# Optimization experiments

Hardware: AMD Instinct MI355X
Metric: run time of the kernel (lower is better)

Reference implementation:

```python
import jax, jax.numpy as jnp
import numpy as np

B, DIM, H, W = 16, 512, 32, 32
C = 256          # internal channels = int(512*0.5)
HEADS = 4        # max(1, 256//64)
KD = 32          # key_dim = int(64*0.5)
HD = 64          # head_dim = 256//4
SCALE = KD ** -0.5


def _silu(x):
    return x * jax.nn.sigmoid(x)


def conv1x1(x, Wm, s, b, act):
    # 1x1 conv + folded eval-mode BN (scale/shift) + optional SiLU
    y = jnp.einsum('bchw,oc->bohw', x, Wm)
    y = y * s[None, :, None, None] + b[None, :, None, None]
    return _silu(y) if act else y


def dwconv3(x, Wd, s, b):
    # depthwise 3x3 conv (groups = channels) + BN scale/shift, no act
    y = jax.lax.conv_general_dilated(
        x, Wd, window_strides=(1, 1), padding='SAME',
        feature_group_count=x.shape[1],
        dimension_numbers=('NCHW', 'OIHW', 'NCHW'))
    return y * s[None, :, None, None] + b[None, :, None, None]


def _mk_conv(key, c_out, c_in, k=1):
    k1, k2, k3 = jax.random.split(key, 3)
    fan_in = c_in * k * k
    if k == 1:
        Wm = jax.random.normal(k1, (c_out, c_in), jnp.float32) * fan_in ** -0.5
    else:
        Wm = jax.random.normal(k1, (c_out, c_in, k, k), jnp.float32) * fan_in ** -0.5
    s = jax.random.uniform(k2, (c_out,), jnp.float32, 0.5, 1.5)
    b = 0.1 * jax.random.normal(k3, (c_out,), jnp.float32)
    return Wm, s, b


def setup_inputs() -> dict:
    key = jax.random.key(0)
    ks = jax.random.split(key, 8)
    x = jax.random.normal(ks[0], (B, DIM, H, W), jnp.float32)
    W_cv1, s_cv1, b_cv1 = _mk_conv(ks[1], 2 * C, DIM)
    W_qkv, s_qkv, b_qkv = _mk_conv(ks[2], C + 2 * HEADS * KD, C)  # 512 out
    W_proj, s_proj, b_proj = _mk_conv(ks[3], C, C)
    # depthwise 3x3: OIHW with I=1, groups=C
    W_pe, s_pe, b_pe = _mk_conv(ks[4], C, 1, k=3)
    W_ffn1, s_ffn1, b_ffn1 = _mk_conv(ks[5], 2 * C, C)
    W_ffn2, s_ffn2, b_ffn2 = _mk_conv(ks[6], C, 2 * C)
    W_cv2, s_cv2, b_cv2 = _mk_conv(ks[7], DIM, 2 * C)
    return {
        'x': x,
        'W_cv1': W_cv1, 's_cv1': s_cv1, 'b_cv1': b_cv1,
        'W_qkv': W_qkv, 's_qkv': s_qkv, 'b_qkv': b_qkv,
        'W_proj': W_proj, 's_proj': s_proj, 'b_proj': b_proj,
        'W_pe': W_pe, 's_pe': s_pe, 'b_pe': b_pe,
        'W_ffn1': W_ffn1, 's_ffn1': s_ffn1, 'b_ffn1': b_ffn1,
        'W_ffn2': W_ffn2, 's_ffn2': s_ffn2, 'b_ffn2': b_ffn2,
        'W_cv2': W_cv2, 's_cv2': s_cv2, 'b_cv2': b_cv2,
    }


def reference(x,
              W_cv1, s_cv1, b_cv1,
              W_qkv, s_qkv, b_qkv,
              W_proj, s_proj, b_proj,
              W_pe, s_pe, b_pe,
              W_ffn1, s_ffn1, b_ffn1,
              W_ffn2, s_ffn2, b_ffn2,
              W_cv2, s_cv2, b_cv2):
    bsz, _, h, w = x.shape
    n = h * w
    y = conv1x1(x, W_cv1, s_cv1, b_cv1, act=True)          # [b, 2C, h, w]
    a, bb = y[:, :C], y[:, C:]

    # ----- Attention on bb -----
    qkv = conv1x1(bb, W_qkv, s_qkv, b_qkv, act=False)       # [b, 2*h*kd + C, h, w]
    qkv = qkv.reshape(bsz, HEADS, 2 * KD + HD, n)
    q, k, v = qkv[:, :, :KD], qkv[:, :, KD:2 * KD], qkv[:, :, 2 * KD:]
    attn = jnp.einsum('bhdn,bhdm->bhnm', q, k) * SCALE      # [b, heads, n, n]
    attn = jax.nn.softmax(attn, axis=-1)
    xa = jnp.einsum('bhdm,bhnm->bhdn', v, attn).reshape(bsz, C, h, w)
    xa = xa + dwconv3(v.reshape(bsz, C, h, w), W_pe, s_pe, b_pe)
    xa = conv1x1(xa, W_proj, s_proj, b_proj, act=False)
    bb = bb + xa

    # ----- FFN on bb -----
    ff = conv1x1(bb, W_ffn1, s_ffn1, b_ffn1, act=True)
    ff = conv1x1(ff, W_ffn2, s_ffn2, b_ffn2, act=False)
    bb = bb + ff

    return conv1x1(jnp.concatenate([a, bb], axis=1), W_cv2, s_cv2, b_cv2, act=True)
```

## Files before the change

kernel.cpp:

```cpp
#include <hip/hip_runtime.h>

typedef unsigned short u16;
typedef __attribute__((ext_vector_type(8))) short short8;
typedef __attribute__((ext_vector_type(4))) float f32x4;
typedef __attribute__((ext_vector_type(4))) unsigned int uint4v;
typedef __attribute__((ext_vector_type(4))) unsigned short ushort4v;

#define N_PIX 1024
constexpr float SCALE = 0.17677669529663687f;
constexpr float QSC   = 0.25506626725324577f;

__device__ __forceinline__ float bf2f(u16 v) {
    unsigned u = ((unsigned)v) << 16;
    return __builtin_bit_cast(float, u);
}
__device__ __forceinline__ u16 f2bf(float f) {
    unsigned u = __builtin_bit_cast(unsigned, f);
    u += 0x7fff + ((u >> 16) & 1);
    return (u16)(u >> 16);
}
__device__ __forceinline__ float silu_f(float x) { return x / (1.f + __expf(-x)); }

__device__ __forceinline__ float exp2_f(float x) {
    float r; asm("v_exp_f32 %0, %1" : "=v"(r) : "v"(x)); return r;
}

__device__ __forceinline__ f32x4 mfma16(short8 a, short8 b, f32x4 c) {
    return __builtin_amdgcn_mfma_f32_16x16x32_bf16(a, b, c, 0, 0, 0);
}

__device__ __forceinline__ void gl_lds16(const u16* g, u16* l) {
    __builtin_amdgcn_global_load_lds(
        (const __attribute__((address_space(1))) unsigned int*)g,
        (__attribute__((address_space(3))) unsigned int*)l, 16, 0, 0);
}

__device__ __forceinline__ float dpp_max16(float x) {
    int v = __builtin_bit_cast(int, x);
    x = fmaxf(x, __builtin_bit_cast(float, __builtin_amdgcn_mov_dpp(v, 0xB1, 0xF, 0xF, true)));
    v = __builtin_bit_cast(int, x);
    x = fmaxf(x, __builtin_bit_cast(float, __builtin_amdgcn_mov_dpp(v, 0x4E, 0xF, 0xF, true)));
    v = __builtin_bit_cast(int, x);
    x = fmaxf(x, __builtin_bit_cast(float, __builtin_amdgcn_mov_dpp(v, 0x141, 0xF, 0xF, true)));
    v = __builtin_bit_cast(int, x);
    x = fmaxf(x, __builtin_bit_cast(float, __builtin_amdgcn_mov_dpp(v, 0x140, 0xF, 0xF, true)));
    return x;
}
__device__ __forceinline__ float dpp_sum16(float x) {
    int v = __builtin_bit_cast(int, x);
    x += __builtin_bit_cast(float, __builtin_amdgcn_mov_dpp(v, 0xB1, 0xF, 0xF, true));
    v = __builtin_bit_cast(int, x);
    x += __builtin_bit_cast(float, __builtin_amdgcn_mov_dpp(v, 0x4E, 0xF, 0xF, true));
    v = __builtin_bit_cast(int, x);
    x += __builtin_bit_cast(float, __builtin_amdgcn_mov_dpp(v, 0x141, 0xF, 0xF, true));
    v = __builtin_bit_cast(int, x);
    x += __builtin_bit_cast(float, __builtin_amdgcn_mov_dpp(v, 0x140, 0xF, 0xF, true));
    return x;
}

__global__ void cvtw_k(const float* s0, u16* d0, int n0,
                       const float* s1, u16* d1, int n1,
                       const float* s2, u16* d2, int n2,
                       const float* s3, u16* d3, int n3,
                       const float* s4, u16* d4, int n4,
                       const float* s5, u16* d5, int n5)
{
    const float* sp = nullptr; u16* dp = nullptr; int n = 0;
    switch (blockIdx.y) {
        case 0: sp = s0; dp = d0; n = n0; break;
        case 1: sp = s1; dp = d1; n = n1; break;
        case 2: sp = s2; dp = d2; n = n2; break;
        case 3: sp = s3; dp = d3; n = n3; break;
        case 4: sp = s4; dp = d4; n = n4; break;
        case 5: sp = s5; dp = d5; n = n5; break;
    }
    for (int i = blockIdx.x * 256 + threadIdx.x; i < n; i += gridDim.x * 256)
        dp[i] = f2bf(sp[i]);
}

__global__ __launch_bounds__(256) void trans_k(const float* __restrict__ x, u16* __restrict__ xt)
{
    __shared__ float LT[64 * 65];
    const int tid = threadIdx.x;
    const int n0 = blockIdx.x * 64;
    const int c0 = blockIdx.y * 64;
    const int b  = blockIdx.z;
    const int w = tid >> 6, ln = tid & 63;
#pragma unroll
    for (int s = 0; s < 16; ++s) {
        int c = s * 4 + w;
        LT[c * 65 + ln] = x[((size_t)(b * 512 + c0 + c)) * N_PIX + n0 + ln];
    }
    __syncthreads();
#pragma unroll
    for (int s = 0; s < 16; ++s) {
        int n = s * 4 + w;
        xt[((size_t)(b * N_PIX + n0 + n)) * 512 + c0 + ln] = f2bf(LT[ln * 65 + n]);
    }
}

__global__ __launch_bounds__(512) void gemm_k(
    const u16* __restrict__ Xt, int xcs, int xcoff,
    const u16* __restrict__ Wb, int Cin,
    const float* __restrict__ sc, const float* __restrict__ bi,
    const u16* __restrict__ res, int rcs, int rcoff,
    u16* __restrict__ out, int ocs, int ocoff,
    float* __restrict__ out32,
    u16* __restrict__ vsep,
    int act)
{
    __shared__ __align__(16) u16 WT[2][128 * 32];
    __shared__ __align__(16) u16 XT[2][128 * 32];
    const int tid  = threadIdx.x;
    const int lane = tid & 63;
    const int w    = __builtin_amdgcn_readfirstlane(tid >> 6);
    const int wr = w & 3;
    const int wc = w >> 2;
    const int n0 = blockIdx.x * 128;
    const int o0 = blockIdx.y * 128;
    const int b  = blockIdx.z;
    const int l4 = lane >> 4, l15 = lane & 15;

    const int srow = tid >> 2;
    const int skc  = (tid & 3) * 8;
    const u16* wg = Wb + (size_t)(o0 + srow) * Cin + skc;
    const u16* xg = Xt + ((size_t)(b * N_PIX + n0 + srow)) * xcs + xcoff + skc;

    f32x4 acc[2][4];
#pragma unroll
    for (int i = 0; i < 2; ++i)
#pragma unroll
        for (int j = 0; j < 4; ++j) acc[i][j] = (f32x4){0.f, 0.f, 0.f, 0.f};

    const int nk = Cin >> 5;
    gl_lds16(wg, &WT[0][tid * 8]);
    gl_lds16(xg, &XT[0][tid * 8]);
    __syncthreads();

    for (int kk = 0; kk < nk; ++kk) {
        const int cur = kk & 1;
        if (kk + 1 < nk) {
            const int cc = (kk + 1) << 5;
            gl_lds16(wg + cc, &WT[cur ^ 1][tid * 8]);
            gl_lds16(xg + cc, &XT[cur ^ 1][tid * 8]);
        }
        short8 af[2], bfr[4];
#pragma unroll
        for (int i = 0; i < 2; ++i)
            af[i] = *(const short8*)&WT[cur][(wr * 32 + i * 16 + l15) * 32 + l4 * 8];
#pragma unroll
        for (int j = 0; j < 4; ++j)
            bfr[j] = *(const short8*)&XT[cur][(wc * 64 + j * 16 + l15) * 32 + l4 * 8];
#pragma unroll
        for (int i = 0; i < 2; ++i)
#pragma unroll
            for (int j = 0; j < 4; ++j)
                acc[i][j] = mfma16(af[i], bfr[j], acc[i][j]);
        __syncthreads();
    }

    if (out32) {
        const int Cout = gridDim.y * 128;
        float* eplds = (float*)XT;
        const int row = tid >> 4, cb = (tid & 15) * 8;
#pragma unroll
        for (int hh = 0; hh < 4; ++hh) {
            if (wr == hh) {
#pragma unroll
                for (int i = 0; i < 2; ++i)
#pragma unroll
                    for (int j = 0; j < 4; ++j)
#pragma unroll
                        for (int r = 0; r < 4; ++r) {
                            const int oo = i * 16 + l4 * 4 + r;
                            const int go = o0 + hh * 32 + oo;
                            float v = acc[i][j][r] * sc[go] + bi[go];
                            if (act) v = silu_f(v);
                            eplds[oo * 128 + wc * 64 + j * 16 + l15] = v;
                        }
            }
            __syncthreads();
            const size_t gidx = ((size_t)b * Cout + o0 + hh * 32 + row) * N_PIX + n0 + cb;
            f32x4 a0 = *(const f32x4*)&eplds[row * 128 + cb];
            f32x4 a1 = *(const f32x4*)&eplds[row * 128 + cb + 4];
            *(f32x4*)&out32[gidx]     = a0;
            *(f32x4*)&out32[gidx + 4] = a1;
            __syncthreads();
        }
        return;
    }

    const bool is_v = (vsep != nullptr) && (wr >= 2);
    const float qmul = (vsep != nullptr && wr == 0) ? QSC : 1.f;
#pragma unroll
    for (int i = 0; i < 2; ++i) {
        const int ob = o0 + wr * 32 + i * 16 + l4 * 4;
        float s4[4], b4[4];
#pragma unroll
        for (int r = 0; r < 4; ++r) { s4[r] = sc[ob + r] * qmul; b4[r] = bi[ob + r] * qmul; }
#pragma unroll
        for (int j = 0; j < 4; ++j) {
            const int n = n0 + wc * 64 + j * 16 + l15;
            float v[4];
#pragma unroll
            for (int r = 0; r < 4; ++r) {
                v[r] = acc[i][j][r] * s4[r] + b4[r];
                if (act) v[r] = silu_f(v[r]);
            }
            if (is_v) {
                const int hh = ob >> 7;
                const int dv = (ob & 127) - 64;
                u16* vp = vsep + (((size_t)(b * 4 + hh)) * 64 + dv) * N_PIX + n;
#pragma unroll
                for (int r = 0; r < 4; ++r) vp[r * N_PIX] = f2bf(v[r]);
            } else {
                const size_t base = ((size_t)(b * N_PIX + n)) * ocs + ocoff + ob;
                if (res) {
                    ushort4v rr = *(const ushort4v*)&res[((size_t)(b * N_PIX + n)) * rcs + rcoff + ob];
#pragma unroll
                    for (int r = 0; r < 4; ++r) v[r] += bf2f(rr[r]);
                }
                ushort4v pk;
#pragma unroll
                for (int r = 0; r < 4; ++r) pk[r] = f2bf(v[r]);
                *(ushort4v*)&out[base] = pk;
            }
        }
    }
}

__global__ __launch_bounds__(256, 4) void attn_k(
    const u16* __restrict__ qkvt, const u16* __restrict__ vsep,
    u16* __restrict__ xat)
{
    __shared__ __align__(16) u16 PL[4 * 16 * 72];
    const int tid  = threadIdx.x;
    const int lane = tid & 63;
    const int w    = __builtin_amdgcn_readfirstlane(tid >> 6);
    const int l4 = lane >> 4, l15 = lane & 15;
    const int h = blockIdx.y, b = blockIdx.z;
    const int n0w = blockIdx.x * 64 + w * 16;
    u16* PLw = PL + w * 16 * 72;

    const short8 qf = *(const short8*)&qkvt[((size_t)(b * N_PIX + n0w + l15)) * 512 + h * 128 + l4 * 8];
    const u16* kb = qkvt + ((size_t)(b * N_PIX + l15)) * 512 + h * 128 + 32 + l4 * 8;
    const u16* vb = vsep + (((size_t)(b * 4 + h)) * 64 + l15) * N_PIX + l4 * 8;

    float mrun[4], lrun[4];
#pragma unroll
    for (int r = 0; r < 4; ++r) { mrun[r] = -1e30f; lrun[r] = 0.f; }
    f32x4 accv[4];
#pragma unroll
    for (int d = 0; d < 4; ++d) accv[d] = (f32x4){0.f, 0.f, 0.f, 0.f};
    const f32x4 z4 = {0.f, 0.f, 0.f, 0.f};

    for (int t = 0; t < 16; ++t) {
        const int m0 = t * 64;
        short8 kf[4];
#pragma unroll
        for (int mt = 0; mt < 4; ++mt)
            kf[mt] = *(const short8*)(kb + (size_t)(m0 + mt * 16) * 512);
        short8 vf[2][4];
#pragma unroll
        for (int mq = 0; mq < 2; ++mq)
#pragma unroll
            for (int d = 0; d < 4; ++d)
                vf[mq][d] = *(const short8*)(vb + (size_t)(d * 16) * N_PIX + m0 + mq * 32);

        f32x4 s[4];
        __builtin_amdgcn_s_setprio(1);
#pragma unroll
        for (int mt = 0; mt < 4; ++mt) s[mt] = mfma16(qf, kf[mt], z4);
        __builtin_amdgcn_s_setprio(0);

        float tm[4], g = -1e30f;
#pragma unroll
        for (int r = 0; r < 4; ++r) {
            float m_ = fmaxf(fmaxf(s[0][r], s[1][r]), fmaxf(s[2][r], s[3][r]));
            tm[r] = dpp_max16(m_);
            g = fmaxf(g, tm[r] - mrun[r]);
        }
        if (!__all(g <= 11.0f)) {
#pragma unroll
            for (int r = 0; r < 4; ++r) {
                float mnew = fmaxf(mrun[r], tm[r]);
                float corr = exp2_f(mrun[r] - mnew);
                mrun[r] = mnew;
                lrun[r] *= corr;
#pragma unroll
                for (int d = 0; d < 4; ++d) accv[d][r] *= corr;
            }
        }
#pragma unroll
        for (int mt = 0; mt < 4; ++mt)
#pragma unroll
            for (int r = 0; r < 4; ++r) {
                float p = exp2_f(s[mt][r] - mrun[r]);
                lrun[r] += p;
                PLw[(l4 * 4 + r) * 72 + mt * 16 + l15] = f2bf(p);
            }

        __builtin_amdgcn_s_setprio(1);
#pragma unroll
        for (int mq = 0; mq < 2; ++mq) {
            short8 pa = *(const short8*)&PLw[l15 * 72 + mq * 32 + l4 * 8];
#pragma unroll
            for (int d = 0; d < 4; ++d)
                accv[d] = mfma16(pa, vf[mq][d], accv[d]);
        }
        __builtin_amdgcn_s_setprio(0);
    }

#pragma unroll
    for (int r = 0; r < 4; ++r)
        lrun[r] = 1.f / dpp_sum16(lrun[r]);
#pragma unroll
    for (int d = 0; d < 4; ++d)
#pragma unroll
        for (int r = 0; r < 4; ++r) {
            const int n = n0w + l4 * 4 + r;
            xat[((size_t)(b * N_PIX + n)) * 256 + h * 64 + d * 16 + l15] =
                f2bf(accv[d][r] * lrun[r]);
        }
}

__global__ __launch_bounds__(256) void pe_k(
    const u16* __restrict__ vsep, const float* __restrict__ Wpe,
    const float* __restrict__ spe, const float* __restrict__ bpe,
    u16* __restrict__ xat)
{
    const int t  = threadIdx.x;
    const int y0 = blockIdx.x * 2;
    const int b  = blockIdx.y;
    const u16* vp = vsep + ((size_t)(b * 256 + t)) * N_PIX;

    float rv[128];
#pragma unroll
    for (int rr = 0; rr < 4; ++rr) {
        const int yy = y0 - 1 + rr;
        if (yy >= 0 && yy < 32) {
#pragma unroll
            for (int g = 0; g < 4; ++g) {
                uint4v u = *(const uint4v*)&vp[yy * 32 + g * 8];
#pragma unroll
                for (int e = 0; e < 4; ++e) {
                    rv[rr * 32 + g * 8 + e * 2]     = bf2f((u16)(u[e] & 0xffff));
                    rv[rr * 32 + g * 8 + e * 2 + 1] = bf2f((u16)(u[e] >> 16));
                }
            }
        } else {
#pragma unroll
            for (int j = 0; j < 32; ++j) rv[rr * 32 + j] = 0.f;
        }
    }
    float w9[9];
#pragma unroll
    for (int i = 0; i < 9; ++i) w9[i] = Wpe[t * 9 + i];
    const float scv = spe[t], biv = bpe[t];
    u16* xp = xat + ((size_t)(b * N_PIX)) * 256 + t;

#pragma unroll
    for (int py = 0; py < 2; ++py)
#pragma unroll
        for (int px = 0; px < 32; ++px) {
            float a = 0.f;
#pragma unroll
            for (int ky = 0; ky < 3; ++ky) {
                const int lr = py + ky;
#pragma unroll
                for (int kx = 0; kx < 3; ++kx) {
                    const int xx = px + kx - 1;
                    if (xx >= 0 && xx < 32)
                        a = fmaf(w9[ky * 3 + kx], rv[lr * 32 + xx], a);
                }
            }
            const int n = (y0 + py) * 32 + px;
            u16* p = xp + (size_t)n * 256;
            *p = f2bf(bf2f(*p) + a * scv + biv);
        }
}

extern "C" void kernel_launch(void* const* d_in, const int* in_sizes, int n_in,
                              void* d_out, int out_size, void* d_ws, size_t ws_size,
                              hipStream_t stream)
{
    const float* x      = (const float*)d_in[0];
    const float* W_cv1  = (const float*)d_in[1];
    const float* s_cv1  = (const float*)d_in[2];
    const float* b_cv1  = (const float*)d_in[3];
    const float* W_qkv  = (const float*)d_in[4];
    const float* s_qkv  = (const float*)d_in[5];
    const float* b_qkv  = (const float*)d_in[6];
    const float* W_proj = (const float*)d_in[7];
    const float* s_proj = (const float*)d_in[8];
    const float* b_proj = (const float*)d_in[9];
    const float* W_pe   = (const float*)d_in[10];
    const float* s_pe   = (const float*)d_in[11];
    const float* b_pe   = (const float*)d_in[12];
    const float* W_ffn1 = (const float*)d_in[13];
    const float* s_ffn1 = (const float*)d_in[14];
    const float* b_ffn1 = (const float*)d_in[15];
    const float* W_ffn2 = (const float*)d_in[16];
    const float* s_ffn2 = (const float*)d_in[17];
    const float* b_ffn2 = (const float*)d_in[18];
    const float* W_cv2  = (const float*)d_in[19];
    const float* s_cv2  = (const float*)d_in[20];
    const float* b_cv2  = (const float*)d_in[21];

    u16* ws = (u16*)d_ws;
    u16* xt      = ws;
    u16* yt      = xt + 8388608;
    u16* qkvt    = yt + 8388608;
    u16* fft     = qkvt + 8388608;
    u16* vsep    = fft + 8388608;
    u16* xat     = vsep + 4194304;
    u16* wb_cv1  = xat + 4194304;
    u16* wb_qkv  = wb_cv1 + 262144;
    u16* wb_proj = wb_qkv + 131072;
    u16* wb_ffn1 = wb_proj + 65536;
    u16* wb_ffn2 = wb_ffn1 + 131072;
    u16* wb_cv2  = wb_ffn2 + 131072;

    cvtw_k<<<dim3(64, 6), 256, 0, stream>>>(
        W_cv1, wb_cv1, 512 * 512, W_qkv, wb_qkv, 512 * 256,
        W_proj, wb_proj, 256 * 256, W_ffn1, wb_ffn1, 512 * 256,
        W_ffn2, wb_ffn2, 256 * 512, W_cv2, wb_cv2, 512 * 512);
    trans_k<<<dim3(16, 8, 16), 256, 0, stream>>>(x, xt);

    gemm_k<<<dim3(8, 4, 16), 512, 0, stream>>>(
        xt, 512, 0, wb_cv1, 512, s_cv1, b_cv1,
        nullptr, 0, 0, yt, 512, 0, nullptr, nullptr, 1);
    gemm_k<<<dim3(8, 4, 16), 512, 0, stream>>>(
        yt, 512, 256, wb_qkv, 256, s_qkv, b_qkv,
        nullptr, 0, 0, qkvt, 512, 0, nullptr, vsep, 0);
    attn_k<<<dim3(16, 4, 16), 256, 0, stream>>>(qkvt, vsep, xat);
    pe_k<<<dim3(16, 16), 256, 0, stream>>>(vsep, W_pe, s_pe, b_pe, xat);
    gemm_k<<<dim3(8, 2, 16), 512, 0, stream>>>(
        xat, 256, 0, wb_proj, 256, s_proj, b_proj,
        yt, 512, 256, yt, 512, 256, nullptr, nullptr, 0);
    gemm_k<<<dim3(8, 4, 16), 512, 0, stream>>>(
        yt, 512, 256, wb_ffn1, 256, s_ffn1, b_ffn1,
        nullptr, 0, 0, fft, 512, 0, nullptr, nullptr, 1);
    gemm_k<<<dim3(8, 2, 16), 512, 0, stream>>>(
        fft, 512, 0, wb_ffn2, 512, s_ffn2, b_ffn2,
        yt, 512, 256, yt, 512, 256, nullptr, nullptr, 0);
    gemm_k<<<dim3(8, 4, 16), 512, 0, stream>>>(
        yt, 512, 0, wb_cv2, 512, s_cv2, b_cv2,
        nullptr, 0, 0, nullptr, 0, 0, (float*)d_out, nullptr, 1);
}
```

Baseline: 320.3 us.

## Triple-buffer GEMM LDS pipeline and stage attention K/V tiles through shared memory

The 1x1-conv GEMM goes from double to triple LDS buffering. It prefetches two K-steps ahead, uses explicit vmcnt waits with raw barriers, and raises wave priority around the MFMA block. The attention kernel no longer has each wave load K/V fragments straight from global memory. Instead the block cooperatively loads each 64-key tile into double-buffered LDS, with register prefetch of the next tile. It also uses a cheaper, non-tie-even bf16 rounding for probabilities and drops the occupancy hint. The aim is better memory latency hiding and less redundant global traffic across waves, at the cost of more LDS use and an extra barrier per tile.

```diff
diff --git a/kernel.cpp b/kernel.cpp
--- a/kernel.cpp
+++ b/kernel.cpp
@@ -7,8 +7,7 @@
 typedef __attribute__((ext_vector_type(4))) unsigned short ushort4v;
 
 #define N_PIX 1024
-constexpr float SCALE = 0.17677669529663687f;
-constexpr float QSC   = 0.25506626725324577f;
+constexpr float QSC = 0.25506626725324577f;
 
 __device__ __forceinline__ float bf2f(u16 v) {
     unsigned u = ((unsigned)v) << 16;
@@ -18,6 +17,10 @@
     unsigned u = __builtin_bit_cast(unsigned, f);
     u += 0x7fff + ((u >> 16) & 1);
     return (u16)(u >> 16);
+}
+__device__ __forceinline__ u16 f2bf_fast(float f) {
+    unsigned u = __builtin_bit_cast(unsigned, f);
+    return (u16)((u + 0x8000u) >> 16);
 }
 __device__ __forceinline__ float silu_f(float x) { return x / (1.f + __expf(-x)); }
 
@@ -109,8 +112,8 @@
     u16* __restrict__ vsep,
     int act)
 {
-    __shared__ __align__(16) u16 WT[2][128 * 32];
-    __shared__ __align__(16) u16 XT[2][128 * 32];
+    __shared__ __align__(16) u16 WT[3][128 * 32];
+    __shared__ __align__(16) u16 XT[3][128 * 32];
     const int tid  = threadIdx.x;
     const int lane = tid & 63;
     const int w    = __builtin_amdgcn_readfirstlane(tid >> 6);
@@ -133,16 +136,26 @@
         for (int j = 0; j < 4; ++j) acc[i][j] = (f32x4){0.f, 0.f, 0.f, 0.f};
 
     const int nk = Cin >> 5;
-    gl_lds16(wg, &WT[0][tid * 8]);
-    gl_lds16(xg, &XT[0][tid * 8]);
-    __syncthreads();
+    gl_lds16(wg,      &WT[0][tid * 8]);
+    gl_lds16(xg,      &XT[0][tid * 8]);
+    gl_lds16(wg + 32, &WT[1][tid * 8]);
+    gl_lds16(xg + 32, &XT[1][tid * 8]);
+    asm volatile("s_waitcnt vmcnt(2)" ::: "memory");
+    __builtin_amdgcn_s_barrier();
+    __builtin_amdgcn_sched_barrier(0);
 
     for (int kk = 0; kk < nk; ++kk) {
-        const int cur = kk & 1;
-        if (kk + 1 < nk) {
-            const int cc = (kk + 1) << 5;
-            gl_lds16(wg + cc, &WT[cur ^ 1][tid * 8]);
-            gl_lds16(xg + cc, &XT[cur ^ 1][tid * 8]);
+        const int cur = kk % 3;
+        if (kk + 2 < nk) {
+            const int cc = (kk + 2) << 5;
+            const int nb = (kk + 2) % 3;
+            gl_lds16(wg + cc, &WT[nb][tid * 8]);
+            gl_lds16(xg + cc, &XT[nb][tid * 8]);
+            asm volatile("s_waitcnt vmcnt(4)" ::: "memory");
+        } else if (kk + 1 < nk) {
+            asm volatile("s_waitcnt vmcnt(2)" ::: "memory");
+        } else {
+            asm volatile("s_waitcnt vmcnt(0)" ::: "memory");
         }
         short8 af[2], bfr[4];
 #pragma unroll
@@ -151,12 +164,15 @@
 #pragma unroll
         for (int j = 0; j < 4; ++j)
             bfr[j] = *(const short8*)&XT[cur][(wc * 64 + j * 16 + l15) * 32 + l4 * 8];
+        __builtin_amdgcn_s_setprio(1);
 #pragma unroll
         for (int i = 0; i < 2; ++i)
 #pragma unroll
             for (int j = 0; j < 4; ++j)
                 acc[i][j] = mfma16(af[i], bfr[j], acc[i][j]);
-        __syncthreads();
+        __builtin_amdgcn_s_setprio(0);
+        __builtin_amdgcn_s_barrier();
+        __builtin_amdgcn_sched_barrier(0);
     }
 
     if (out32) {
@@ -229,10 +245,12 @@
     }
 }
 
-__global__ __launch_bounds__(256, 4) void attn_k(
+__global__ __launch_bounds__(256) void attn_k(
     const u16* __restrict__ qkvt, const u16* __restrict__ vsep,
     u16* __restrict__ xat)
 {
+    __shared__ __align__(16) u16 KT[2][64 * 40];
+    __shared__ __align__(16) u16 VT[2][64 * 72];
     __shared__ __align__(16) u16 PL[4 * 16 * 72];
     const int tid  = threadIdx.x;
     const int lane = tid & 63;
@@ -243,8 +261,11 @@
     u16* PLw = PL + w * 16 * 72;
 
     const short8 qf = *(const short8*)&qkvt[((size_t)(b * N_PIX + n0w + l15)) * 512 + h * 128 + l4 * 8];
-    const u16* kb = qkvt + ((size_t)(b * N_PIX + l15)) * 512 + h * 128 + 32 + l4 * 8;
-    const u16* vb = vsep + (((size_t)(b * 4 + h)) * 64 + l15) * N_PIX + l4 * 8;
+
+    const int skr = tid >> 2, skc = (tid & 3) * 8;
+    const int svd = tid >> 3, svm = (tid & 7) * 8;
+    const u16* kgbase = qkvt + ((size_t)(b * N_PIX + skr)) * 512 + h * 128 + 32 + skc;
+    const u16* vgbase = vsep + (((size_t)(b * 4 + h)) * 64 + svd) * N_PIX + svm;
 
     float mrun[4], lrun[4];
 #pragma unroll
@@ -254,23 +275,30 @@
     for (int d = 0; d < 4; ++d) accv[d] = (f32x4){0.f, 0.f, 0.f, 0.f};
     const f32x4 z4 = {0.f, 0.f, 0.f, 0.f};
 
+    uint4v kreg = *(const uint4v*)(kgbase);
+    uint4v vr0  = *(const uint4v*)(vgbase);
+    uint4v vr1  = *(const uint4v*)(vgbase + 32 * N_PIX);
+
     for (int t = 0; t < 16; ++t) {
-        const int m0 = t * 64;
-        short8 kf[4];
-#pragma unroll
-        for (int mt = 0; mt < 4; ++mt)
-            kf[mt] = *(const short8*)(kb + (size_t)(m0 + mt * 16) * 512);
-        short8 vf[2][4];
-#pragma unroll
-        for (int mq = 0; mq < 2; ++mq)
-#pragma unroll
-            for (int d = 0; d < 4; ++d)
-                vf[mq][d] = *(const short8*)(vb + (size_t)(d * 16) * N_PIX + m0 + mq * 32);
+        const int cur = t & 1;
+        *(uint4v*)&KT[cur][skr * 40 + skc] = kreg;
+        *(uint4v*)&VT[cur][svd * 72 + svm] = vr0;
+        *(uint4v*)&VT[cur][(svd + 32) * 72 + svm] = vr1;
+        if (t < 15) {
+            const int m1 = (t + 1) * 64;
+            kreg = *(const uint4v*)(kgbase + (size_t)m1 * 512);
+            vr0  = *(const uint4v*)(vgbase + m1);
+            vr1  = *(const uint4v*)(vgbase + 32 * N_PIX + m1);
+        }
+        __syncthreads();
 
         f32x4 s[4];
         __builtin_amdgcn_s_setprio(1);
 #pragma unroll
-        for (int mt = 0; mt < 4; ++mt) s[mt] = mfma16(qf, kf[mt], z4);
+        for (int mt = 0; mt < 4; ++mt) {
+            short8 kf = *(const short8*)&KT[cur][(mt * 16 + l15) * 40 + l4 * 8];
+            s[mt] = mfma16(qf, kf, z4);
+        }
         __builtin_amdgcn_s_setprio(0);
 
         float tm[4], g = -1e30f;
@@ -297,7 +325,7 @@
             for (int r = 0; r < 4; ++r) {
                 float p = exp2_f(s[mt][r] - mrun[r]);
                 lrun[r] += p;
-                PLw[(l4 * 4 + r) * 72 + mt * 16 + l15] = f2bf(p);
+                PLw[(l4 * 4 + r) * 72 + mt * 16 + l15] = f2bf_fast(p);
             }
 
         __builtin_amdgcn_s_setprio(1);
@@ -305,8 +333,10 @@
         for (int mq = 0; mq < 2; ++mq) {
             short8 pa = *(const short8*)&PLw[l15 * 72 + mq * 32 + l4 * 8];
 #pragma unroll
-            for (int d = 0; d < 4; ++d)
-                accv[d] = mfma16(pa, vf[mq][d], accv[d]);
+            for (int d = 0; d < 4; ++d) {
+                short8 vf = *(const short8*)&VT[cur][(d * 16 + l15) * 72 + mq * 32 + l4 * 8];
+                accv[d] = mfma16(pa, vf, accv[d]);
+            }
         }
         __builtin_amdgcn_s_setprio(0);
     }
```

Result: faster. 268.4 us (-16.2%).
